# Optimization experiments

Hardware: AMD Instinct MI355X
Metric: run time of the kernel (lower is better)

## Reference

```python
import jax, jax.numpy as jnp
import numpy as np

B, S, D = 4, 8192, 64
N_HASHES = 8
BUCKET_SIZE = 64
N_BUCKETS = S // BUCKET_SIZE  # 128, must be even


def setup_inputs() -> dict:
    key = jax.random.key(0)
    k1, k2, k3 = jax.random.split(key, 3)
    qk = jax.random.normal(k1, (B, S, D), dtype=jnp.float32)
    v = jax.random.normal(k2, (B, S, D), dtype=jnp.float32)
    # random rotations for LSH hashing (source draws these with tf.random.normal each call)
    rotations = jax.random.normal(k3, (1, D, N_HASHES, N_BUCKETS // 2), dtype=jnp.float32)
    return {"qk": qk, "v": v, "rotations": rotations}


def _lsh_attention(qk, v, rotations, bucket_size=BUCKET_SIZE, n_hashes=N_HASHES):
    b, s, d = qk.shape
    n_buckets = s // bucket_size
    # ---- hash_vectors (rehash_each_round=True path) ----
    rot = jnp.broadcast_to(rotations, (b,) + rotations.shape[1:])  # (b, d, h, n_buckets//2)
    rotated = jnp.einsum('btf,bfhi->bhti', qk, rot)                # (b, h, s, n_buckets//2)
    rotated = jnp.concatenate([rotated, -rotated], axis=-1)        # (b, h, s, n_buckets)
    buckets = jnp.argmax(rotated, axis=-1)                         # (b, h, s)
    offsets = (jnp.arange(n_hashes) * n_buckets).reshape(1, -1, 1)
    buckets = (buckets + offsets).reshape(b, -1)                   # (b, h*s), in [0, h*n_buckets)

    # ---- sort by (bucket, position) ----
    total = n_hashes * s
    ticker = jnp.arange(total)
    buckets_and_t = s * buckets + (ticker % s)[None, :]            # (b, h*s)
    sticker = jnp.argsort(buckets_and_t, axis=-1)                  # sorted order (ticker values)
    undo_sort = jnp.argsort(sticker, axis=-1)

    st = sticker % s                                               # original seq positions
    sqk = jnp.take_along_axis(qk, st[:, :, None], axis=1)          # (b, h*s, d)
    sv = jnp.take_along_axis(v, st[:, :, None], axis=1)

    # ---- chunk into n_hashes*n_buckets bins of size bucket_size ----
    c = n_hashes * n_buckets
    bq_t = st.reshape(b, c, -1)                                    # (b, c, m)
    bqk = sqk.reshape(b, c, -1, d)
    bv = sv.reshape(b, c, -1, v.shape[-1])
    bq = bqk
    bk = bqk / (jnp.linalg.norm(bqk, axis=-1, keepdims=True) + 1e-6)

    def look_one_back(x):
        extra = jnp.concatenate([x[:, -1:], x[:, :-1]], axis=1)
        return jnp.concatenate([x, extra], axis=2)

    bk = look_one_back(bk)
    bv = look_one_back(bv)
    bkv_t = look_one_back(bq_t)

    dots = jnp.einsum('bhie,bhje->bhij', bq, bk) * (d ** -0.5)     # (b, c, m, 2m)
    # faithful to source: dots = dots*mask + (1-mask)*(-1e5) with mask = (bq_t == bkv_t)
    self_mask = bq_t[:, :, :, None] == bkv_t[:, :, None, :]
    dots = jnp.where(self_mask, dots, jnp.float32(-1e5))

    lse = jax.nn.logsumexp(dots, axis=-1, keepdims=True)
    probs = jnp.exp(dots - lse)
    bo = jnp.einsum('buij,buje->buie', probs, bv)                  # (b, c, m, dv)
    so = bo.reshape(b, -1, bo.shape[-1])                           # (b, h*s, dv)
    slogits = lse.reshape(b, -1)                                   # (b, h*s)

    # ---- unsort ----
    o = jnp.take_along_axis(so, undo_sort[:, :, None], axis=1)
    logits = jnp.take_along_axis(slogits, undo_sort, axis=1)

    # ---- combine hash rounds by logit-weighted average ----
    o = o.reshape(b, n_hashes, s, -1)
    logits = logits.reshape(b, n_hashes, s, 1)
    w = jnp.exp(logits - jax.nn.logsumexp(logits, axis=1, keepdims=True))
    out = jnp.sum(o * w, axis=1)                                   # (b, s, dv)
    return out, buckets


def reference(qk, v, rotations):
    return _lsh_attention(qk, v, rotations)
```

## Files before the change

### kernel.cpp

```cpp
#include <hip/hip_runtime.h>


namespace {
constexpr int S_LEN   = 8192;
constexpr int D_DIM   = 64;
constexpr int N_HASH  = 8;
constexpr int N_BUCK  = 128;
constexpr int T_TILE  = 128;
constexpr int THREADS = 256;
constexpr int BATCH   = 4;
constexpr int H_PER   = 2;
constexpr int BSTRIDE = 72;
constexpr float MARGIN = 8e-3f;
constexpr long long OUT0_ELEMS = (long long)BATCH * S_LEN * D_DIM;
}

typedef __attribute__((ext_vector_type(8))) short bf16x8;
typedef __attribute__((ext_vector_type(4))) float f32x4;
typedef __attribute__((ext_vector_type(4))) unsigned uint4v;

__device__ __forceinline__ unsigned pack_hi16(unsigned u0, unsigned u1) {
  return __builtin_amdgcn_perm(u1, u0, 0x07060302u);
}

__global__ __launch_bounds__(THREADS, 4) void lsh_mfma_kernel(
    const float* __restrict__ qk, const float* __restrict__ v,
    const float* __restrict__ rot, float* __restrict__ out) {
  const int b    = blockIdx.z;
  const int hb   = blockIdx.y;
  const int tile = blockIdx.x;
  const int tid  = threadIdx.x;
  const int wave = tid >> 6;
  const int lane = tid & 63;
  const int col  = lane & 15;
  const int quad = lane >> 4;

  __shared__ __align__(16) unsigned short lbh[H_PER][64 * BSTRIDE];
  __shared__ __align__(16) unsigned short lbl[H_PER][64 * BSTRIDE];
  __shared__ int s_cnt;
  __shared__ int s_list[H_PER * T_TILE];
  if (tid == 0) s_cnt = 0;

  {
    const int bid = blockIdx.x + gridDim.x * (blockIdx.y + gridDim.y * blockIdx.z);
    const int base = bid * 512 + tid;
    ((float4*)out)[base]       = ((const float4*)v)[base];
    ((float4*)out)[base + 256] = ((const float4*)v)[base + 256];
  }

  {
    const int n  = tid >> 2;
    const int k0 = (tid & 3) * 16;
#pragma unroll
    for (int hh = 0; hh < H_PER; ++hh) {
      const float* rp = rot + (hb * H_PER + hh) * 64 + n;
      unsigned hu[8], lu[8];
#pragma unroll
      for (int p = 0; p < 8; ++p) {
        const float x0 = rp[(size_t)(k0 + 2 * p) * 512];
        const float x1 = rp[(size_t)(k0 + 2 * p + 1) * 512];
        const unsigned u0 = __float_as_uint(x0);
        const unsigned u1 = __float_as_uint(x1);
        const float l0 = x0 - __uint_as_float(u0 & 0xffff0000u);
        const float l1 = x1 - __uint_as_float(u1 & 0xffff0000u);
        hu[p] = pack_hi16(u0, u1);
        lu[p] = pack_hi16(__float_as_uint(l0), __float_as_uint(l1));
      }
      const int off = n * BSTRIDE + k0;
      *(uint4v*)&lbh[hh][off]     = uint4v{hu[0], hu[1], hu[2], hu[3]};
      *(uint4v*)&lbh[hh][off + 8] = uint4v{hu[4], hu[5], hu[6], hu[7]};
      *(uint4v*)&lbl[hh][off]     = uint4v{lu[0], lu[1], lu[2], lu[3]};
      *(uint4v*)&lbl[hh][off + 8] = uint4v{lu[4], lu[5], lu[6], lu[7]};
    }
  }
  __syncthreads();

  const int trow0 = tile * T_TILE + wave * 32;
  bf16x8 Ah[2][2], Al[2][2];
#pragma unroll
  for (int mt = 0; mt < 2; ++mt) {
    const float* qrow = qk + ((size_t)b * S_LEN + trow0 + mt * 16 + col) * D_DIM;
#pragma unroll
    for (int kk = 0; kk < 2; ++kk) {
      float qb[8];
      *(float4*)qb       = *(const float4*)(qrow + kk * 32 + quad * 8);
      *(float4*)(qb + 4) = *(const float4*)(qrow + kk * 32 + quad * 8 + 4);
      unsigned hu[4], lu[4];
#pragma unroll
      for (int p = 0; p < 4; ++p) {
        const unsigned u0 = __float_as_uint(qb[2 * p]);
        const unsigned u1 = __float_as_uint(qb[2 * p + 1]);
        const float l0 = qb[2 * p]     - __uint_as_float(u0 & 0xffff0000u);
        const float l1 = qb[2 * p + 1] - __uint_as_float(u1 & 0xffff0000u);
        hu[p] = pack_hi16(u0, u1);
        lu[p] = pack_hi16(__float_as_uint(l0), __float_as_uint(l1));
      }
      Ah[mt][kk] = __builtin_bit_cast(bf16x8, uint4v{hu[0], hu[1], hu[2], hu[3]});
      Al[mt][kk] = __builtin_bit_cast(bf16x8, uint4v{lu[0], lu[1], lu[2], lu[3]});
    }
  }

  const int basec0 = 127 - col;

#pragma unroll
  for (int hh = 0; hh < H_PER; ++hh) {
    const int h = hb * H_PER + hh;
    bf16x8 Bh[4][2];
#pragma unroll
    for (int nt = 0; nt < 4; ++nt)
#pragma unroll
      for (int kk = 0; kk < 2; ++kk)
        Bh[nt][kk] =
            *(const bf16x8*)&lbh[hh][(nt * 16 + col) * BSTRIDE + kk * 32 + quad * 8];

    float* outb = out + OUT0_ELEMS + ((size_t)(b * N_HASH + h)) * S_LEN + tile * T_TILE;

#pragma unroll
    for (int mt = 0; mt < 2; ++mt) {
      f32x4 acc[4];
#pragma unroll
      for (int nt = 0; nt < 4; ++nt) {
        f32x4 c = {0.f, 0.f, 0.f, 0.f};
#pragma unroll
        for (int kk = 0; kk < 2; ++kk) {
          const bf16x8 bl =
              *(const bf16x8*)&lbl[hh][(nt * 16 + col) * BSTRIDE + kk * 32 + quad * 8];
          c = __builtin_amdgcn_mfma_f32_16x16x32_bf16(Ah[mt][kk], Bh[nt][kk], c, 0, 0, 0);
          c = __builtin_amdgcn_mfma_f32_16x16x32_bf16(Ah[mt][kk], bl, c, 0, 0, 0);
          c = __builtin_amdgcn_mfma_f32_16x16x32_bf16(Al[mt][kk], Bh[nt][kk], c, 0, 0, 0);
        }
        acc[nt] = c;
      }

#pragma unroll
      for (int reg = 0; reg < 4; ++reg) {
        unsigned m1 = 0u, m2 = 0u;
#pragma unroll
        for (int nt = 0; nt < 4; ++nt) {
          const unsigned u = __float_as_uint(acc[nt][reg]);
          const unsigned a = u & 0x7fffffffu;
          const unsigned code = (unsigned)(basec0 - nt * 16) - ((u >> 25) & 0x40u);
          const unsigned key = (a & 0xffffff80u) | code;
          const unsigned t = min(m1, key);
          m2 = max(m2, t);
          m1 = max(m1, key);
        }
#pragma unroll
        for (int m = 1; m < 16; m <<= 1) {
          const unsigned o1 = (unsigned)__shfl_xor((int)m1, m);
          const unsigned o2 = (unsigned)__shfl_xor((int)m2, m);
          const unsigned t = min(m1, o1);
          m2 = max(max(m2, o2), t);
          m1 = max(m1, o1);
        }
        if (col == 0) {
          const float v1 = __uint_as_float(m1 & 0xffffff80u);
          const float v2 = __uint_as_float(m2 & 0xffffff80u);
          const int t_local = wave * 32 + mt * 16 + quad * 4 + reg;
          if (v1 - v2 < MARGIN) {
            s_list[atomicAdd(&s_cnt, 1)] = (hh << 8) | t_local;
          } else {
            const int idx = 127 - (int)(m1 & 0x7fu);
            outb[t_local] = (float)(idx + h * N_BUCK);
          }
        }
      }
    }
  }

  __syncthreads();

  const int cnt = s_cnt;
  for (int it = wave; it < cnt; it += THREADS / 64) {
    const int e  = s_list[it];
    const int hh = e >> 8;
    const int tl = e & 255;
    const int h  = hb * H_PER + hh;
    const float* qrow = qk + ((size_t)b * S_LEN + tile * T_TILE + tl) * D_DIM;
    double dot = 0.0;
#pragma unroll 8
    for (int f = 0; f < D_DIM; ++f)
      dot = fma((double)qrow[f], (double)rot[(size_t)f * 512 + h * 64 + lane], dot);
    double vp = dot, vn = -dot;
    int ip = lane, in_ = 64 + lane;
#pragma unroll
    for (int m = 1; m < 64; m <<= 1) {
      const double ovp = __shfl_xor(vp, m);
      const int   oip = __shfl_xor(ip, m);
      if (ovp > vp || (ovp == vp && oip < ip)) { vp = ovp; ip = oip; }
      const double ovn = __shfl_xor(vn, m);
      const int   oin = __shfl_xor(in_, m);
      if (ovn > vn || (ovn == vn && oin < in_)) { vn = ovn; in_ = oin; }
    }
    if (lane == 0) {
      const int bucket = (vp >= vn) ? ip : in_;
      out[OUT0_ELEMS + ((size_t)(b * N_HASH + h)) * S_LEN + tile * T_TILE + tl] =
          (float)(bucket + h * N_BUCK);
    }
  }
}

extern "C" void kernel_launch(void* const* d_in, const int* in_sizes, int n_in,
                              void* d_out, int out_size, void* d_ws, size_t ws_size,
                              hipStream_t stream) {
  const float* qk  = (const float*)d_in[0];
  const float* v   = (const float*)d_in[1];
  const float* rot = (const float*)d_in[2];
  float* out = (float*)d_out;

  dim3 grid(S_LEN / T_TILE, N_HASH / H_PER, BATCH);
  lsh_mfma_kernel<<<grid, THREADS, 0, stream>>>(qk, v, rot, out);
}
```

Before: 84.77 us.

## Replace shared-memory fallback list with per-wave ballot masks and reorder loads

Rows whose top-two bucket scores fall within the margin are now recorded in per-wave register bitmasks built with ballot, instead of an atomic-appended shared list. This removes the second block-wide barrier and the shared atomics, and each wave rechecks only its own rows in double precision. The qk row loads are hoisted ahead of the rotation staging so their latency overlaps the shared-memory setup, and the v copy-through moves to the end of the kernel. The trade-off is worse load balance when ambiguous rows cluster in one wave, plus extra registers to hold the qk rows.

```diff
diff --git a/kernel.cpp b/kernel.cpp
--- a/kernel.cpp
+++ b/kernel.cpp
@@ -37,15 +37,17 @@
 
   __shared__ __align__(16) unsigned short lbh[H_PER][64 * BSTRIDE];
   __shared__ __align__(16) unsigned short lbl[H_PER][64 * BSTRIDE];
-  __shared__ int s_cnt;
-  __shared__ int s_list[H_PER * T_TILE];
-  if (tid == 0) s_cnt = 0;
-
-  {
-    const int bid = blockIdx.x + gridDim.x * (blockIdx.y + gridDim.y * blockIdx.z);
-    const int base = bid * 512 + tid;
-    ((float4*)out)[base]       = ((const float4*)v)[base];
-    ((float4*)out)[base + 256] = ((const float4*)v)[base + 256];
+
+  const int trow0 = tile * T_TILE + wave * 32;
+  float qb[2][2][8];
+#pragma unroll
+  for (int mt = 0; mt < 2; ++mt) {
+    const float* qrow = qk + ((size_t)b * S_LEN + trow0 + mt * 16 + col) * D_DIM;
+#pragma unroll
+    for (int kk = 0; kk < 2; ++kk) {
+      *(float4*)&qb[mt][kk][0] = *(const float4*)(qrow + kk * 32 + quad * 8);
+      *(float4*)&qb[mt][kk][4] = *(const float4*)(qrow + kk * 32 + quad * 8 + 4);
+    }
   }
 
   {
@@ -75,23 +77,20 @@
   }
   __syncthreads();
 
-  const int trow0 = tile * T_TILE + wave * 32;
   bf16x8 Ah[2][2], Al[2][2];
 #pragma unroll
   for (int mt = 0; mt < 2; ++mt) {
-    const float* qrow = qk + ((size_t)b * S_LEN + trow0 + mt * 16 + col) * D_DIM;
 #pragma unroll
     for (int kk = 0; kk < 2; ++kk) {
-      float qb[8];
-      *(float4*)qb       = *(const float4*)(qrow + kk * 32 + quad * 8);
-      *(float4*)(qb + 4) = *(const float4*)(qrow + kk * 32 + quad * 8 + 4);
       unsigned hu[4], lu[4];
 #pragma unroll
       for (int p = 0; p < 4; ++p) {
-        const unsigned u0 = __float_as_uint(qb[2 * p]);
-        const unsigned u1 = __float_as_uint(qb[2 * p + 1]);
-        const float l0 = qb[2 * p]     - __uint_as_float(u0 & 0xffff0000u);
-        const float l1 = qb[2 * p + 1] - __uint_as_float(u1 & 0xffff0000u);
+        const float x0 = qb[mt][kk][2 * p];
+        const float x1 = qb[mt][kk][2 * p + 1];
+        const unsigned u0 = __float_as_uint(x0);
+        const unsigned u1 = __float_as_uint(x1);
+        const float l0 = x0 - __uint_as_float(u0 & 0xffff0000u);
+        const float l1 = x1 - __uint_as_float(u1 & 0xffff0000u);
         hu[p] = pack_hi16(u0, u1);
         lu[p] = pack_hi16(__float_as_uint(l0), __float_as_uint(l1));
       }
@@ -101,6 +100,7 @@
   }
 
   const int basec0 = 127 - col;
+  unsigned rmask[H_PER] = {0u, 0u};
 
 #pragma unroll
   for (int hh = 0; hh < H_PER; ++hh) {
@@ -153,50 +153,67 @@
           m2 = max(max(m2, o2), t);
           m1 = max(m1, o1);
         }
+        bool amb = false;
         if (col == 0) {
           const float v1 = __uint_as_float(m1 & 0xffffff80u);
           const float v2 = __uint_as_float(m2 & 0xffffff80u);
-          const int t_local = wave * 32 + mt * 16 + quad * 4 + reg;
-          if (v1 - v2 < MARGIN) {
-            s_list[atomicAdd(&s_cnt, 1)] = (hh << 8) | t_local;
-          } else {
+          amb = (v1 - v2 < MARGIN);
+          if (!amb) {
+            const int t_local = wave * 32 + mt * 16 + quad * 4 + reg;
             const int idx = 127 - (int)(m1 & 0x7fu);
             outb[t_local] = (float)(idx + h * N_BUCK);
           }
         }
-      }
-    }
-  }
-
-  __syncthreads();
-
-  const int cnt = s_cnt;
-  for (int it = wave; it < cnt; it += THREADS / 64) {
-    const int e  = s_list[it];
-    const int hh = e >> 8;
-    const int tl = e & 255;
-    const int h  = hb * H_PER + hh;
-    const float* qrow = qk + ((size_t)b * S_LEN + tile * T_TILE + tl) * D_DIM;
-    double dot = 0.0;
+        const unsigned long long bal = __ballot(amb);
+        if (bal) {
+          const unsigned q0 = (unsigned)(bal & 1ull);
+          const unsigned q1 = (unsigned)((bal >> 16) & 1ull);
+          const unsigned q2 = (unsigned)((bal >> 32) & 1ull);
+          const unsigned q3 = (unsigned)((bal >> 48) & 1ull);
+          const unsigned spread = q0 | (q1 << 4) | (q2 << 8) | (q3 << 12);
+          rmask[hh] |= spread << (mt * 16 + reg);
+        }
+      }
+    }
+  }
+
+#pragma unroll
+  for (int hh = 0; hh < H_PER; ++hh) {
+    unsigned m = rmask[hh];
+    const int h = hb * H_PER + hh;
+    while (m) {
+      const int row = __builtin_ctz(m);
+      m &= m - 1;
+      const int tl = wave * 32 + row;
+      const float* qrow = qk + ((size_t)b * S_LEN + tile * T_TILE + tl) * D_DIM;
+      double dot = 0.0;
 #pragma unroll 8
-    for (int f = 0; f < D_DIM; ++f)
-      dot = fma((double)qrow[f], (double)rot[(size_t)f * 512 + h * 64 + lane], dot);
-    double vp = dot, vn = -dot;
-    int ip = lane, in_ = 64 + lane;
-#pragma unroll
-    for (int m = 1; m < 64; m <<= 1) {
-      const double ovp = __shfl_xor(vp, m);
-      const int   oip = __shfl_xor(ip, m);
-      if (ovp > vp || (ovp == vp && oip < ip)) { vp = ovp; ip = oip; }
-      const double ovn = __shfl_xor(vn, m);
-      const int   oin = __shfl_xor(in_, m);
-      if (ovn > vn || (ovn == vn && oin < in_)) { vn = ovn; in_ = oin; }
-    }
-    if (lane == 0) {
-      const int bucket = (vp >= vn) ? ip : in_;
-      out[OUT0_ELEMS + ((size_t)(b * N_HASH + h)) * S_LEN + tile * T_TILE + tl] =
-          (float)(bucket + h * N_BUCK);
-    }
+      for (int f = 0; f < D_DIM; ++f)
+        dot = fma((double)qrow[f], (double)rot[(size_t)f * 512 + h * 64 + lane], dot);
+      double vp = dot, vn = -dot;
+      int ip = lane, in_ = 64 + lane;
+#pragma unroll
+      for (int s = 1; s < 64; s <<= 1) {
+        const double ovp = __shfl_xor(vp, s);
+        const int   oip = __shfl_xor(ip, s);
+        if (ovp > vp || (ovp == vp && oip < ip)) { vp = ovp; ip = oip; }
+        const double ovn = __shfl_xor(vn, s);
+        const int   oin = __shfl_xor(in_, s);
+        if (ovn > vn || (ovn == vn && oin < in_)) { vn = ovn; in_ = oin; }
+      }
+      if (lane == 0) {
+        const int bucket = (vp >= vn) ? ip : in_;
+        out[OUT0_ELEMS + ((size_t)(b * N_HASH + h)) * S_LEN + tile * T_TILE + tl] =
+            (float)(bucket + h * N_BUCK);
+      }
+    }
+  }
+
+  {
+    const int bid = blockIdx.x + gridDim.x * (blockIdx.y + gridDim.y * blockIdx.z);
+    const int base = bid * 512 + tid;
+    ((float4*)out)[base]       = ((const float4*)v)[base];
+    ((float4*)out)[base + 256] = ((const float4*)v)[base + 256];
   }
 }
 
```

Measured after the change: 87.59 us. +3.3%, slower.
